# Kernel optimization log

Hardware: AMD Instinct MI355X
Metric: run time of the kernel (lower is better)

Reference implementation:

```python
import jax, jax.numpy as jnp
import numpy as np

H = 1024        # hidden_dim
NH = 8          # num_heads
HD = H // NH    # head_dim
EPS = 1e-5


def setup_inputs() -> dict:
    key = jax.random.key(0)
    ks = jax.random.split(key, 16)
    s = 0.02
    d = {
        'x': jax.random.normal(ks[0], (2, 2048, H), dtype=jnp.float32),
        'ln1_g': jnp.ones((H,), jnp.float32), 'ln1_b': jnp.zeros((H,), jnp.float32),
        'ln2_g': jnp.ones((H,), jnp.float32), 'ln2_b': jnp.zeros((H,), jnp.float32),
        'Wq': jax.random.normal(ks[1], (H, H), jnp.float32) * s,
        'bq': jnp.zeros((H,), jnp.float32),
        'Wk': jax.random.normal(ks[2], (H, H), jnp.float32) * s,
        'bk': jnp.zeros((H,), jnp.float32),
        'Wv': jax.random.normal(ks[3], (H, H), jnp.float32) * s,
        'bv': jnp.zeros((H,), jnp.float32),
        'Wo': jax.random.normal(ks[4], (H, H), jnp.float32) * s,
        'bo': jnp.zeros((H,), jnp.float32),
        'W1': jax.random.normal(ks[5], (H, 4 * H), jnp.float32) * s,
        'b1': jnp.zeros((4 * H,), jnp.float32),
        'W2': jax.random.normal(ks[6], (4 * H, H), jnp.float32) * s,
        'b2': jnp.zeros((H,), jnp.float32),
    }
    return d


def _layernorm(x, g, b):
    mu = jnp.mean(x, axis=-1, keepdims=True)
    var = jnp.mean(jnp.square(x - mu), axis=-1, keepdims=True)
    return (x - mu) * jax.lax.rsqrt(var + EPS) * g + b


def _block(x, ln1_g, ln1_b, ln2_g, ln2_b, Wq, bq, Wk, bk, Wv, bv, Wo, bo, W1, b1, W2, b2):
    B, S, _ = x.shape
    h = _layernorm(x, ln1_g, ln1_b)
    q = (h @ Wq + bq).reshape(B, S, NH, HD).transpose(0, 2, 1, 3)  # [B,NH,S,HD]
    k = (h @ Wk + bk).reshape(B, S, NH, HD).transpose(0, 2, 1, 3)
    v = (h @ Wv + bv).reshape(B, S, NH, HD).transpose(0, 2, 1, 3)
    scores = jnp.einsum('bhqd,bhkd->bhqk', q, k) / np.sqrt(HD)
    causal = jnp.tril(jnp.ones((S, S), bool))
    scores = jnp.where(causal, scores, -jnp.inf)
    attn = jax.nn.softmax(scores, axis=-1)
    y = jnp.einsum('bhqk,bhkd->bhqd', attn, v).transpose(0, 2, 1, 3).reshape(B, S, H)
    x = x + y @ Wo + bo
    h2 = _layernorm(x, ln2_g, ln2_b)
    m = jax.nn.gelu(h2 @ W1 + b1, approximate=False) @ W2 + b2
    return x + m


def reference(x, ln1_g, ln1_b, ln2_g, ln2_b, Wq, bq, Wk, bk, Wv, bv, Wo, bo, W1, b1, W2, b2):
    return _block(x, ln1_g, ln1_b, ln2_g, ln2_b, Wq, bq, Wk, bk, Wv, bv, Wo, bo, W1, b1, W2, b2)
```

## Files before the change

kernel.cpp:

```cpp
#include <hip/hip_runtime.h>
#include <hip/hip_bf16.h>
#include <math.h>

using bf16 = __hip_bfloat16;
typedef __attribute__((ext_vector_type(8))) short short8v;
typedef __attribute__((ext_vector_type(4))) float f32x4;

#define DEV __device__ __forceinline__

DEV void load_lds16(const bf16* gsrc, bf16* ldst) {
  __builtin_amdgcn_global_load_lds((const __attribute__((address_space(1))) void*)gsrc,
                                   (__attribute__((address_space(3))) void*)ldst, 16, 0, 0);
}

DEV void swz8(int& bx, int& by, int gx, int gy) {
  const int n = gx * gy, c = n >> 3;
  int lin = bx + gx * by;
  lin = (lin & 7) * c + (lin >> 3);
  bx = lin % gx; by = lin / gx;
}

__global__ __launch_bounds__(256) void prep_kernel(
    const float* __restrict__ Wq, const float* __restrict__ Wk, const float* __restrict__ Wv,
    const float* __restrict__ Wo, const float* __restrict__ W1, const float* __restrict__ W2,
    bf16* __restrict__ WqT, bf16* __restrict__ WkT, bf16* __restrict__ WvT,
    bf16* __restrict__ WoT, bf16* __restrict__ W1T, bf16* __restrict__ W2T,
    const float* __restrict__ x, const float* __restrict__ ln1g, const float* __restrict__ ln1b,
    bf16* __restrict__ h) {
  __shared__ float tile[64][65];
  const int b = blockIdx.x;
  if (b >= 3072) {
    const int row = b - 3072, t = threadIdx.x;
    const float4 v = ((const float4*)(x + (size_t)row * 1024))[t];
    float s = v.x + v.y + v.z + v.w;
#pragma unroll
    for (int mm = 1; mm < 64; mm <<= 1) s += __shfl_xor(s, mm);
    __shared__ float r1[4], r2[4];
    if ((t & 63) == 0) r1[t >> 6] = s;
    __syncthreads();
    const float mean = (r1[0] + r1[1] + r1[2] + r1[3]) * (1.0f / 1024.0f);
    const float d0 = v.x - mean, d1 = v.y - mean, d2 = v.z - mean, d3 = v.w - mean;
    float s2 = d0 * d0 + d1 * d1 + d2 * d2 + d3 * d3;
#pragma unroll
    for (int mm = 1; mm < 64; mm <<= 1) s2 += __shfl_xor(s2, mm);
    if ((t & 63) == 0) r2[t >> 6] = s2;
    __syncthreads();
    const float var = (r2[0] + r2[1] + r2[2] + r2[3]) * (1.0f / 1024.0f);
    const float rinv = rsqrtf(var + 1e-5f);
    const int c = t * 4;
    bf16* o = h + (size_t)row * 1024 + c;
    o[0] = __float2bfloat16(d0 * rinv * ln1g[c + 0] + ln1b[c + 0]);
    o[1] = __float2bfloat16(d1 * rinv * ln1g[c + 1] + ln1b[c + 1]);
    o[2] = __float2bfloat16(d2 * rinv * ln1g[c + 2] + ln1b[c + 2]);
    o[3] = __float2bfloat16(d3 * rinv * ln1g[c + 3] + ln1b[c + 3]);
    return;
  }
  const float* W; bf16* WT; int K, N, n0, k0;
  if (b < 1024) {
    const int which = b >> 8, t = b & 255;
    W  = (which == 0) ? Wq  : (which == 1) ? Wk  : (which == 2) ? Wv  : Wo;
    WT = (which == 0) ? WqT : (which == 1) ? WkT : (which == 2) ? WvT : WoT;
    K = 1024; N = 1024; n0 = (t & 15) * 64; k0 = (t >> 4) * 64;
  } else if (b < 2048) {
    const int t = b - 1024;
    W = W1; WT = W1T; K = 1024; N = 4096; n0 = (t & 63) * 64; k0 = (t >> 6) * 64;
  } else {
    const int t = b - 2048;
    W = W2; WT = W2T; K = 4096; N = 1024; n0 = (t & 15) * 64; k0 = (t >> 4) * 64;
  }
  const int tx = threadIdx.x & 15, ty = threadIdx.x >> 4;
#pragma unroll
  for (int p = 0; p < 4; ++p) {
    int r = p * 16 + ty;
    float4 vv = *(const float4*)&W[(size_t)(k0 + r) * N + n0 + tx * 4];
    tile[r][tx * 4 + 0] = vv.x; tile[r][tx * 4 + 1] = vv.y;
    tile[r][tx * 4 + 2] = vv.z; tile[r][tx * 4 + 3] = vv.w;
  }
  __syncthreads();
#pragma unroll
  for (int p = 0; p < 4; ++p) {
    int n = p * 16 + ty;
    bf16* dst = WT + (size_t)(n0 + n) * K + k0 + tx * 4;
#pragma unroll
    for (int j = 0; j < 4; ++j) dst[j] = __float2bfloat16(tile[tx * 4 + j][n]);
  }
}

__global__ __launch_bounds__(256) void ln_kernel(const float* __restrict__ x,
                                                 const float* __restrict__ g,
                                                 const float* __restrict__ b,
                                                 bf16* __restrict__ out) {
  const int row = blockIdx.x, t = threadIdx.x;
  const float4 v = ((const float4*)(x + (size_t)row * 1024))[t];
  float s = v.x + v.y + v.z + v.w;
#pragma unroll
  for (int mm = 1; mm < 64; mm <<= 1) s += __shfl_xor(s, mm);
  __shared__ float r1[4], r2[4];
  if ((t & 63) == 0) r1[t >> 6] = s;
  __syncthreads();
  const float mean = (r1[0] + r1[1] + r1[2] + r1[3]) * (1.0f / 1024.0f);
  const float d0 = v.x - mean, d1 = v.y - mean, d2 = v.z - mean, d3 = v.w - mean;
  float s2 = d0 * d0 + d1 * d1 + d2 * d2 + d3 * d3;
#pragma unroll
  for (int mm = 1; mm < 64; mm <<= 1) s2 += __shfl_xor(s2, mm);
  if ((t & 63) == 0) r2[t >> 6] = s2;
  __syncthreads();
  const float var = (r2[0] + r2[1] + r2[2] + r2[3]) * (1.0f / 1024.0f);
  const float rinv = rsqrtf(var + 1e-5f);
  const int c = t * 4;
  bf16* o = out + (size_t)row * 1024 + c;
  o[0] = __float2bfloat16(d0 * rinv * g[c + 0] + b[c + 0]);
  o[1] = __float2bfloat16(d1 * rinv * g[c + 1] + b[c + 1]);
  o[2] = __float2bfloat16(d2 * rinv * g[c + 2] + b[c + 2]);
  o[3] = __float2bfloat16(d3 * rinv * g[c + 3] + b[c + 3]);
}

template <int EPI>
__global__ __launch_bounds__(512, 2) void gemm256(
    const bf16* __restrict__ A, const bf16* __restrict__ BT,
    const float* __restrict__ bias0, const float* __restrict__ bias1, const float* __restrict__ bias2,
    void* __restrict__ outp, int M, int N, int K) {
  __shared__ bf16 As[4][256 * 32];
  __shared__ bf16 Bs[4][256 * 32];
  const int tid = threadIdx.x;
  const int w = tid >> 6, l = tid & 63;
  const int wm = w >> 2, wn = w & 3;
  const int c = l & 15, h4 = l >> 4;
  int bx = blockIdx.x, by = blockIdx.y;
  swz8(bx, by, gridDim.x, gridDim.y);
  const int m0 = by * 256, n0 = bx * 256;

  const float* bias;
  int zz = 0;
  if (EPI == 0) {
    zz = n0 >> 10;
    bias = ((zz == 0) ? bias0 : (zz == 1) ? bias1 : bias2) - (zz << 10);
  } else {
    bias = bias0;
  }

  const int rl = l >> 2;
  const int ch = (l & 3) * 8;
  const int nkt = K >> 5;

  f32x4 acc[8][4] = {};

  auto STAGE_A = [&](int t, int b) {
    const bf16* src = A + (size_t)(m0 + rl) * K + t * 32 + ch;
    load_lds16(src + (size_t)((w * 2 + 0) * 16) * K, &As[b][(w * 2 + 0) * 512]);
    load_lds16(src + (size_t)((w * 2 + 1) * 16) * K, &As[b][(w * 2 + 1) * 512]);
  };
  auto STAGE_B = [&](int t, int b) {
    const bf16* src = BT + (size_t)(n0 + rl) * K + t * 32 + ch;
    load_lds16(src + (size_t)((w * 2 + 0) * 16) * K, &Bs[b][(w * 2 + 0) * 512]);
    load_lds16(src + (size_t)((w * 2 + 1) * 16) * K, &Bs[b][(w * 2 + 1) * 512]);
  };

  STAGE_A(0, 0); STAGE_B(0, 0);
  STAGE_A(1, 1); STAGE_B(1, 1);
  STAGE_A(2, 2); STAGE_B(2, 2);
  asm volatile("s_waitcnt vmcnt(8)" ::: "memory");
  __builtin_amdgcn_sched_barrier(0);
  __builtin_amdgcn_s_barrier();

  for (int t = 0; t < nkt; ++t) {
    const bf16* Ab = &As[t & 3][0];
    const bf16* Bb = &Bs[t & 3][0];
    short8v a[4], b[4];
#pragma unroll
    for (int i = 0; i < 4; ++i)
      a[i] = *(const short8v*)&Ab[(wm * 128 + i * 16 + c) * 32 + h4 * 8];
#pragma unroll
    for (int i = 0; i < 4; ++i)
      b[i] = *(const short8v*)&Bb[(wn * 64 + i * 16 + c) * 32 + h4 * 8];
    if (t + 3 < nkt) STAGE_A(t + 3, (t + 3) & 3);
    asm volatile("s_waitcnt lgkmcnt(0)" ::: "memory");
    __builtin_amdgcn_sched_barrier(0);
    __builtin_amdgcn_s_setprio(1);
#pragma unroll
    for (int mi = 0; mi < 4; ++mi)
#pragma unroll
      for (int ni = 0; ni < 4; ++ni)
        acc[mi][ni] = __builtin_amdgcn_mfma_f32_16x16x32_bf16(a[mi], b[ni], acc[mi][ni], 0, 0, 0);
    __builtin_amdgcn_s_setprio(0);
#pragma unroll
    for (int i = 0; i < 4; ++i)
      a[i] = *(const short8v*)&Ab[(wm * 128 + 64 + i * 16 + c) * 32 + h4 * 8];
    if (t + 3 < nkt) STAGE_B(t + 3, (t + 3) & 3);
    asm volatile("s_waitcnt lgkmcnt(0)" ::: "memory");
    __builtin_amdgcn_sched_barrier(0);
    __builtin_amdgcn_s_setprio(1);
#pragma unroll
    for (int mi = 0; mi < 4; ++mi)
#pragma unroll
      for (int ni = 0; ni < 4; ++ni)
        acc[4 + mi][ni] = __builtin_amdgcn_mfma_f32_16x16x32_bf16(a[mi], b[ni], acc[4 + mi][ni], 0, 0, 0);
    __builtin_amdgcn_s_setprio(0);
    if (t < nkt - 3)       asm volatile("s_waitcnt vmcnt(8)" ::: "memory");
    else if (t == nkt - 3) asm volatile("s_waitcnt vmcnt(4)" ::: "memory");
    else                   asm volatile("s_waitcnt vmcnt(0)" ::: "memory");
    __builtin_amdgcn_sched_barrier(0);
    __builtin_amdgcn_s_barrier();
  }

#pragma unroll
  for (int mi = 0; mi < 8; ++mi) {
#pragma unroll
    for (int ni = 0; ni < 4; ++ni) {
#pragma unroll
      for (int r = 0; r < 4; ++r) {
        const int m = m0 + wm * 128 + mi * 16 + h4 * 4 + r;
        const int n = n0 + wn * 64 + ni * 16 + c;
        const float vv = acc[mi][ni][r] + bias[n];
        if (EPI == 0) {
          const int bb = m >> 11, ss = m & 2047;
          const int n1 = n - (zz << 10);
          const int hh = n1 >> 7, dd = n1 & 127;
          ((bf16*)outp)[(size_t)zz * 4194304 + (((size_t)bb * 8 + hh) * 2048 + ss) * 128 + dd] =
              __float2bfloat16(vv);
        } else {
          const size_t idx = (size_t)m * N + n;
          const float u = 0.7978845608028654f * (vv + 0.044715f * vv * vv * vv);
          const float tt = __expf(2.0f * u);
          const float th = 1.0f - 2.0f / (tt + 1.0f);
          ((bf16*)outp)[idx] = __float2bfloat16(0.5f * vv * (1.0f + th));
        }
      }
    }
  }
}

template <int EPI, int MI>
__global__ __launch_bounds__(256) void gemm128(
    const bf16* __restrict__ A, const bf16* __restrict__ BT,
    const float* __restrict__ bias0, const float* __restrict__ bias1, const float* __restrict__ bias2,
    const float* __restrict__ res, void* __restrict__ outp,
    int M, int N, int K) {
  __shared__ bf16 As[2][MI * 1024];
  __shared__ bf16 Bs[2][128 * 32];
  const int tid = threadIdx.x;
  const int w = tid >> 6, l = tid & 63;
  const int wr = w >> 1, wc = w & 1;
  const int col = l & 15, hi = l >> 4;
  int bx = blockIdx.x, by = blockIdx.y;
  swz8(bx, by, gridDim.x, gridDim.y);
  const int m0 = by * (32 * MI), n0 = bx * 128;

  const float* bias = bias0;

  const int srow = l >> 2;
  const int scol = ((l & 3) ^ ((l >> 4) & 3)) * 8;
  const int rs = col * 4 + (hi ^ ((l >> 2) & 3));
  f32x4 acc[MI][4] = {};

  const int nk = K >> 5;
#pragma unroll
  for (int j = 0; j < MI / 2; ++j) {
    const int grp = w * (MI / 2) + j;
    load_lds16(A + (size_t)(m0 + grp * 16 + srow) * K + scol, &As[0][grp * 512]);
  }
#pragma unroll
  for (int j = 0; j < 2; ++j) {
    const int grp = w * 2 + j;
    load_lds16(BT + (size_t)(n0 + grp * 16 + srow) * K + scol, &Bs[0][grp * 512]);
  }
  __syncthreads();

  int cur = 0;
  for (int kt = 0; kt < nk; ++kt) {
    if (kt + 1 < nk) {
      const int k0n = (kt + 1) * 32;
#pragma unroll
      for (int j = 0; j < MI / 2; ++j) {
        const int grp = w * (MI / 2) + j;
        load_lds16(A + (size_t)(m0 + grp * 16 + srow) * K + k0n + scol, &As[cur ^ 1][grp * 512]);
      }
#pragma unroll
      for (int j = 0; j < 2; ++j) {
        const int grp = w * 2 + j;
        load_lds16(BT + (size_t)(n0 + grp * 16 + srow) * K + k0n + scol, &Bs[cur ^ 1][grp * 512]);
      }
    }
    __builtin_amdgcn_sched_barrier(0);

    short8v af[MI], bfr[4];
#pragma unroll
    for (int i = 0; i < MI; ++i)
      af[i] = *(const short8v*)&As[cur][(wr * MI + i) * 512 + rs * 8];
#pragma unroll
    for (int i = 0; i < 4; ++i)
      bfr[i] = *(const short8v*)&Bs[cur][(wc * 4 + i) * 512 + rs * 8];
#pragma unroll
    for (int mi = 0; mi < MI; ++mi)
#pragma unroll
      for (int ni = 0; ni < 4; ++ni)
        acc[mi][ni] = __builtin_amdgcn_mfma_f32_16x16x32_bf16(af[mi], bfr[ni], acc[mi][ni], 0, 0, 0);
    __syncthreads();
    cur ^= 1;
  }

#pragma unroll
  for (int mi = 0; mi < MI; ++mi) {
#pragma unroll
    for (int ni = 0; ni < 4; ++ni) {
#pragma unroll
      for (int r = 0; r < 4; ++r) {
        const int m = m0 + wr * (16 * MI) + mi * 16 + hi * 4 + r;
        const int n = n0 + wc * 64 + ni * 16 + col;
        const float vv = acc[mi][ni][r] + bias[n];
        const size_t idx = (size_t)m * N + n;
        ((float*)outp)[idx] = res[idx] + vv;
      }
    }
  }
}

__global__ __launch_bounds__(512) void gemm_sk(
    const bf16* __restrict__ A, const bf16* __restrict__ BT,
    const float* __restrict__ bias, const float* __restrict__ res, float* __restrict__ outp,
    int M, int N, int K) {
  __shared__ bf16 As[2][2][4096];
  __shared__ bf16 Bs[2][2][4096];
  __shared__ float dump[128 * 132];
  const int tid = threadIdx.x;
  const int w = tid >> 6, l = tid & 63;
  const int grp = w >> 2, wg = w & 3;
  const int wr = wg >> 1, wc = wg & 1;
  const int col = l & 15, hi = l >> 4;
  int bx = blockIdx.x, by = blockIdx.y;
  swz8(bx, by, gridDim.x, gridDim.y);
  const int m0 = by * 128, n0 = bx * 128;

  const int srow = l >> 2;
  const int scol = ((l & 3) ^ ((l >> 4) & 3)) * 8;
  const int rs = col * 4 + (hi ^ ((l >> 2) & 3));
  f32x4 acc[4][4] = {};

  const int KH = K >> 1;
  const int kbase = grp * KH;
  const int nk = KH >> 5;

#pragma unroll
  for (int j = 0; j < 2; ++j) {
    const int rg = wg * 2 + j;
    load_lds16(A + (size_t)(m0 + rg * 16 + srow) * K + kbase + scol, &As[grp][0][rg * 512]);
    load_lds16(BT + (size_t)(n0 + rg * 16 + srow) * K + kbase + scol, &Bs[grp][0][rg * 512]);
  }
  __syncthreads();

  int cur = 0;
  for (int kt = 0; kt < nk; ++kt) {
    if (kt + 1 < nk) {
      const int k0n = kbase + (kt + 1) * 32;
#pragma unroll
      for (int j = 0; j < 2; ++j) {
        const int rg = wg * 2 + j;
        load_lds16(A + (size_t)(m0 + rg * 16 + srow) * K + k0n + scol, &As[grp][cur ^ 1][rg * 512]);
        load_lds16(BT + (size_t)(n0 + rg * 16 + srow) * K + k0n + scol, &Bs[grp][cur ^ 1][rg * 512]);
      }
    }
    __builtin_amdgcn_sched_barrier(0);

    short8v af[4], bfr[4];
#pragma unroll
    for (int i = 0; i < 4; ++i) {
      af[i]  = *(const short8v*)&As[grp][cur][(wr * 4 + i) * 512 + rs * 8];
      bfr[i] = *(const short8v*)&Bs[grp][cur][(wc * 4 + i) * 512 + rs * 8];
    }
#pragma unroll
    for (int mi = 0; mi < 4; ++mi)
#pragma unroll
      for (int ni = 0; ni < 4; ++ni)
        acc[mi][ni] = __builtin_amdgcn_mfma_f32_16x16x32_bf16(af[mi], bfr[ni], acc[mi][ni], 0, 0, 0);
    __syncthreads();
    cur ^= 1;
  }

  if (grp == 1) {
#pragma unroll
    for (int mi = 0; mi < 4; ++mi)
#pragma unroll
      for (int ni = 0; ni < 4; ++ni)
#pragma unroll
        for (int r = 0; r < 4; ++r)
          dump[(wr * 64 + mi * 16 + hi * 4 + r) * 132 + wc * 64 + ni * 16 + col] = acc[mi][ni][r];
  }
  __syncthreads();
  if (grp == 0) {
#pragma unroll
    for (int mi = 0; mi < 4; ++mi) {
#pragma unroll
      for (int ni = 0; ni < 4; ++ni) {
#pragma unroll
        for (int r = 0; r < 4; ++r) {
          const int lrow = wr * 64 + mi * 16 + hi * 4 + r;
          const int lcol = wc * 64 + ni * 16 + col;
          const int m = m0 + lrow, n = n0 + lcol;
          const size_t idx = (size_t)m * N + n;
          outp[idx] = res[idx] + acc[mi][ni][r] + dump[lrow * 132 + lcol] + bias[n];
        }
      }
    }
  }
}

__global__ __launch_bounds__(512) void attn_kernel(const bf16* __restrict__ q,
                                                   const bf16* __restrict__ k,
                                                   const bf16* __restrict__ v,
                                                   bf16* __restrict__ y) {
  __shared__ __align__(16) char lds_raw[157696];
  int p = blockIdx.x, bh = blockIdx.y;
  swz8(p, bh, 16, 16);
  const int tid = threadIdx.x;
  const int w = tid >> 6, l = tid & 63;
  const int grp = w >> 2, wg = w & 3;
  const int col = l & 15, hi = l >> 4;

  const bf16* kbase = k + (size_t)bh * 2048 * 128;
  const bf16* vbase = v + (size_t)bh * 2048 * 128;
  const int bb = bh >> 3, hh = bh & 7;

  bf16* Psw = (bf16*)(lds_raw + 139264 + (size_t)w * 2304);

  const int klr = (l >> 4);
  const int kblk0 = l & 15;
  const int vr = (l & 31) * 2;
  const int vcb = (wg * 2 + (l >> 5)) * 16;

  const float scale = 0.08838834764831845f;

  for (int half = 0; half < 2; ++half) {
    const int qt = half ? p : (31 - p);
    const int q0 = qt * 64;
    const int T = qt + 1;
    const int n0 = (T + 1) >> 1;
    const int myn = grp ? (T >> 1) : n0;
    const int tb = grp ? n0 : 0;

    short8v qf[4];
    const bf16* qp = q + ((size_t)bh * 2048 + q0 + wg * 16 + col) * 128;
#pragma unroll
    for (int c = 0; c < 4; ++c) qf[c] = *(const short8v*)(qp + c * 32 + hi * 8);

    f32x4 o[8] = {};
    float mx[4] = {-1e30f, -1e30f, -1e30f, -1e30f};
    float sm[4] = {0.f, 0.f, 0.f, 0.f};

    if (myn > 0) {
      bf16* Ks0 = (bf16*)(lds_raw + (size_t)(grp * 2 + 0) * 16384);
      bf16* Vt0 = (bf16*)(lds_raw + 65536 + (size_t)(grp * 2 + 0) * 18432);
#pragma unroll
      for (int j = 0; j < 4; ++j) {
        const int lr = j * 4 + klr;
        const int blk = kblk0 ^ (lr & 7);
        load_lds16(kbase + (size_t)(tb * 64 + wg * 16 + lr) * 128 + blk * 8,
                   Ks0 + wg * 2048 + j * 512);
      }
      const bf16* vsrc = vbase + (size_t)(tb * 64 + vr) * 128 + vcb;
      short8v v00 = *(const short8v*)vsrc;
      short8v v01 = *(const short8v*)(vsrc + 8);
      short8v v10 = *(const short8v*)(vsrc + 128);
      short8v v11 = *(const short8v*)(vsrc + 136);
#pragma unroll
      for (int i = 0; i < 8; ++i) {
        *(unsigned int*)&Vt0[(vcb + i) * 72 + vr] =
            ((unsigned int)(unsigned short)v00[i]) | (((unsigned int)(unsigned short)v10[i]) << 16);
        *(unsigned int*)&Vt0[(vcb + 8 + i) * 72 + vr] =
            ((unsigned int)(unsigned short)v01[i]) | (((unsigned int)(unsigned short)v11[i]) << 16);
      }
    }
    __syncthreads();

    for (int it = 0; it < n0; ++it) {
      const int cur = it & 1;
      const bool active = it < myn;
      const bool havenext = (it + 1) < myn;
      bf16* KsCur = (bf16*)(lds_raw + (size_t)(grp * 2 + cur) * 16384);
      bf16* KsNxt = (bf16*)(lds_raw + (size_t)(grp * 2 + (cur ^ 1)) * 16384);
      bf16* VtCur = (bf16*)(lds_raw + 65536 + (size_t)(grp * 2 + cur) * 18432);
      bf16* VtNxt = (bf16*)(lds_raw + 65536 + (size_t)(grp * 2 + (cur ^ 1)) * 18432);

      short8v v00, v01, v10, v11;
      if (havenext) {
        const int nt = tb + it + 1;
#pragma unroll
        for (int j = 0; j < 4; ++j) {
          const int lr = j * 4 + klr;
          const int blk = kblk0 ^ (lr & 7);
          load_lds16(kbase + (size_t)(nt * 64 + wg * 16 + lr) * 128 + blk * 8,
                     KsNxt + wg * 2048 + j * 512);
        }
        const bf16* vsrc = vbase + (size_t)(nt * 64 + vr) * 128 + vcb;
        v00 = *(const short8v*)vsrc;
        v01 = *(const short8v*)(vsrc + 8);
        v10 = *(const short8v*)(vsrc + 128);
        v11 = *(const short8v*)(vsrc + 136);
      }

      if (active) {
        const int ktile = tb + it;
        f32x4 s[4] = {};
        __builtin_amdgcn_s_setprio(1);
#pragma unroll
        for (int c = 0; c < 4; ++c) {
#pragma unroll
          for (int kg = 0; kg < 4; ++kg) {
            const int kr = kg * 16 + col;
            short8v kf = *(const short8v*)&KsCur[kr * 128 + ((c * 32 + hi * 8) ^ ((col & 7) << 3))];
            s[kg] = __builtin_amdgcn_mfma_f32_16x16x32_bf16(qf[c], kf, s[kg], 0, 0, 0);
          }
        }
        __builtin_amdgcn_s_setprio(0);

        const bool diag = (ktile == qt);
        const int qrl = wg * 16 + hi * 4;
        float al[4];
#pragma unroll
        for (int r = 0; r < 4; ++r) {
          float a0 = s[0][r] * scale, a1 = s[1][r] * scale;
          float a2 = s[2][r] * scale, a3 = s[3][r] * scale;
          if (diag) {
            const int qr = qrl + r;
            if (0 * 16 + col > qr) a0 = -1e30f;
            if (1 * 16 + col > qr) a1 = -1e30f;
            if (2 * 16 + col > qr) a2 = -1e30f;
            if (3 * 16 + col > qr) a3 = -1e30f;
          }
          float t = fmaxf(fmaxf(a0, a1), fmaxf(a2, a3));
#pragma unroll
          for (int mm = 1; mm < 16; mm <<= 1) t = fmaxf(t, __shfl_xor(t, mm));
          const float mn = fmaxf(mx[r], t);
          const float aa = __expf(mx[r] - mn);
          const float p0 = __expf(a0 - mn), p1 = __expf(a1 - mn);
          const float p2 = __expf(a2 - mn), p3 = __expf(a3 - mn);
          float ps = (p0 + p1) + (p2 + p3);
#pragma unroll
          for (int mm = 1; mm < 16; mm <<= 1) ps += __shfl_xor(ps, mm);
          sm[r] = sm[r] * aa + ps;
          mx[r] = mn; al[r] = aa;
          const int prow = (hi * 4 + r) * 72;
          Psw[prow + col]      = __float2bfloat16(p0);
          Psw[prow + col + 16] = __float2bfloat16(p1);
          Psw[prow + col + 32] = __float2bfloat16(p2);
          Psw[prow + col + 48] = __float2bfloat16(p3);
        }
#pragma unroll
        for (int db = 0; db < 8; ++db)
#pragma unroll
          for (int r = 0; r < 4; ++r) o[db][r] *= al[r];
      }

      if (havenext) {
#pragma unroll
        for (int i = 0; i < 8; ++i) {
          *(unsigned int*)&VtNxt[(vcb + i) * 72 + vr] =
              ((unsigned int)(unsigned short)v00[i]) | (((unsigned int)(unsigned short)v10[i]) << 16);
          *(unsigned int*)&VtNxt[(vcb + 8 + i) * 72 + vr] =
              ((unsigned int)(unsigned short)v01[i]) | (((unsigned int)(unsigned short)v11[i]) << 16);
        }
      }

      if (active) {
        asm volatile("s_waitcnt lgkmcnt(0)" ::: "memory");
        __builtin_amdgcn_s_setprio(1);
#pragma unroll
        for (int ks = 0; ks < 2; ++ks) {
          short8v pf = *(const short8v*)&Psw[col * 72 + ks * 32 + hi * 8];
#pragma unroll
          for (int db = 0; db < 8; ++db) {
            short8v vf = *(const short8v*)&VtCur[(db * 16 + col) * 72 + ks * 32 + hi * 8];
            o[db] = __builtin_amdgcn_mfma_f32_16x16x32_bf16(pf, vf, o[db], 0, 0, 0);
          }
        }
        __builtin_amdgcn_s_setprio(0);
      }
      __syncthreads();
    }

    if (grp == 1) {
      float* Mo = (float*)(lds_raw + (size_t)wg * 8448);
      float* Ml = (float*)(lds_raw + 33792 + (size_t)wg * 128);
#pragma unroll
      for (int db = 0; db < 8; ++db)
#pragma unroll
        for (int r = 0; r < 4; ++r)
          Mo[(hi * 4 + r) * 132 + db * 16 + col] = o[db][r];
#pragma unroll
      for (int r = 0; r < 4; ++r) {
        Ml[(hi * 4 + r) * 2 + 0] = mx[r];
        Ml[(hi * 4 + r) * 2 + 1] = sm[r];
      }
    }
    __syncthreads();
    if (grp == 0) {
      const float* Mo = (const float*)(lds_raw + (size_t)wg * 8448);
      const float* Ml = (const float*)(lds_raw + 33792 + (size_t)wg * 128);
      float a0[4], a1[4], inv[4];
#pragma unroll
      for (int r = 0; r < 4; ++r) {
        const float m1 = Ml[(hi * 4 + r) * 2 + 0];
        const float l1 = Ml[(hi * 4 + r) * 2 + 1];
        const float M = fmaxf(mx[r], m1);
        a0[r] = __expf(mx[r] - M);
        a1[r] = __expf(m1 - M);
        inv[r] = 1.0f / (sm[r] * a0[r] + l1 * a1[r]);
      }
#pragma unroll
      for (int db = 0; db < 8; ++db) {
#pragma unroll
        for (int r = 0; r < 4; ++r) {
          const float oc = o[db][r] * a0[r] + Mo[(hi * 4 + r) * 132 + db * 16 + col] * a1[r];
          const int qg = q0 + wg * 16 + hi * 4 + r;
          y[((size_t)bb * 2048 + qg) * 1024 + hh * 128 + db * 16 + col] =
              __float2bfloat16(oc * inv[r]);
        }
      }
    }
    __syncthreads();
  }
}

extern "C" void kernel_launch(void* const* d_in, const int* in_sizes, int n_in,
                              void* d_out, int out_size, void* d_ws, size_t ws_size,
                              hipStream_t stream) {
  const float* x    = (const float*)d_in[0];
  const float* ln1g = (const float*)d_in[1];
  const float* ln1b = (const float*)d_in[2];
  const float* ln2g = (const float*)d_in[3];
  const float* ln2b = (const float*)d_in[4];
  const float* Wq   = (const float*)d_in[5];
  const float* bq   = (const float*)d_in[6];
  const float* Wk   = (const float*)d_in[7];
  const float* bk   = (const float*)d_in[8];
  const float* Wv   = (const float*)d_in[9];
  const float* bv   = (const float*)d_in[10];
  const float* Wo   = (const float*)d_in[11];
  const float* bo   = (const float*)d_in[12];
  const float* W1   = (const float*)d_in[13];
  const float* b1   = (const float*)d_in[14];
  const float* W2   = (const float*)d_in[15];
  const float* b2   = (const float*)d_in[16];
  float* out = (float*)d_out;
  char* ws = (char*)d_ws;
  const size_t MB = 1024 * 1024;

  bf16* WqT = (bf16*)(ws + 0 * MB);
  bf16* WkT = (bf16*)(ws + 2 * MB);
  bf16* WvT = (bf16*)(ws + 4 * MB);
  bf16* WoT = (bf16*)(ws + 6 * MB);
  bf16* W1T = (bf16*)(ws + 8 * MB);
  bf16* W2T = (bf16*)(ws + 16 * MB);
  bf16* h   = (bf16*)(ws + 24 * MB);
  bf16* qb  = (bf16*)(ws + 32 * MB);
  bf16* kb  = (bf16*)(ws + 40 * MB);
  bf16* vb  = (bf16*)(ws + 48 * MB);
  bf16* y   = (bf16*)(ws + 56 * MB);
  bf16* g   = (bf16*)(ws + 32 * MB);
  float* x1 = (float*)(ws + 64 * MB);
  bf16* h2  = h;

  prep_kernel<<<7168, 256, 0, stream>>>(Wq, Wk, Wv, Wo, W1, W2, WqT, WkT, WvT, WoT, W1T, W2T,
                                        x, ln1g, ln1b, h);

  gemm256<0><<<dim3(12, 16), 512, 0, stream>>>(h, WqT, bq, bk, bv, qb, 4096, 3072, 1024);

  attn_kernel<<<dim3(16, 16), 512, 0, stream>>>(qb, kb, vb, y);

  gemm128<1, 2><<<dim3(8, 64), 256, 0, stream>>>(y, WoT, bo, nullptr, nullptr, x, x1,
                                                 4096, 1024, 1024);

  ln_kernel<<<4096, 256, 0, stream>>>(x1, ln2g, ln2b, h2);

  gemm256<2><<<dim3(16, 16), 512, 0, stream>>>(h2, W1T, b1, nullptr, nullptr, g,
                                               4096, 4096, 1024);

  gemm_sk<<<dim3(8, 32), 512, 0, stream>>>(g, W2T, b2, x1, out, 4096, 1024, 4096);
}
```

Baseline: 256.2 us.

## Deepen W2 split-K GEMM pipeline to four LDS stages with manual waitcnts

Rewrites the split-K down-projection GEMM so each K-group prefetches three tiles ahead into a four-deep LDS ring. Explicit vmcnt/lgkmcnt waits and raw s_barrier replace the per-iteration __syncthreads, and MFMA sections run at raised wave priority. The goal is to hide global-load latency better. In exchange it drops the XOR swizzle on LDS tiles, which may add bank conflicts, and uses 128KB of LDS, limiting occupancy to one block per CU.

```diff
diff --git a/kernel.cpp b/kernel.cpp
--- a/kernel.cpp
+++ b/kernel.cpp
@@ -315,13 +315,11 @@
   }
 }
 
-__global__ __launch_bounds__(512) void gemm_sk(
+__global__ __launch_bounds__(512, 1) void gemm_sk2(
     const bf16* __restrict__ A, const bf16* __restrict__ BT,
     const float* __restrict__ bias, const float* __restrict__ res, float* __restrict__ outp,
     int M, int N, int K) {
-  __shared__ bf16 As[2][2][4096];
-  __shared__ bf16 Bs[2][2][4096];
-  __shared__ float dump[128 * 132];
+  __shared__ __align__(16) char lds_raw[131072];
   const int tid = threadIdx.x;
   const int w = tid >> 6, l = tid & 63;
   const int grp = w >> 2, wg = w & 3;
@@ -331,51 +329,59 @@
   swz8(bx, by, gridDim.x, gridDim.y);
   const int m0 = by * 128, n0 = bx * 128;
 
-  const int srow = l >> 2;
-  const int scol = ((l & 3) ^ ((l >> 4) & 3)) * 8;
-  const int rs = col * 4 + (hi ^ ((l >> 2) & 3));
+  const int rl = l >> 2;
+  const int ch = (l & 3) * 8;
   f32x4 acc[4][4] = {};
 
   const int KH = K >> 1;
   const int kbase = grp * KH;
-  const int nk = KH >> 5;
-
-#pragma unroll
-  for (int j = 0; j < 2; ++j) {
-    const int rg = wg * 2 + j;
-    load_lds16(A + (size_t)(m0 + rg * 16 + srow) * K + kbase + scol, &As[grp][0][rg * 512]);
-    load_lds16(BT + (size_t)(n0 + rg * 16 + srow) * K + kbase + scol, &Bs[grp][0][rg * 512]);
-  }
-  __syncthreads();
-
-  int cur = 0;
-  for (int kt = 0; kt < nk; ++kt) {
-    if (kt + 1 < nk) {
-      const int k0n = kbase + (kt + 1) * 32;
-#pragma unroll
-      for (int j = 0; j < 2; ++j) {
-        const int rg = wg * 2 + j;
-        load_lds16(A + (size_t)(m0 + rg * 16 + srow) * K + k0n + scol, &As[grp][cur ^ 1][rg * 512]);
-        load_lds16(BT + (size_t)(n0 + rg * 16 + srow) * K + k0n + scol, &Bs[grp][cur ^ 1][rg * 512]);
-      }
-    }
+  const int nkt = KH >> 5;
+
+  auto ABUF = [&](int b) { return (bf16*)(lds_raw + grp * 65536 + b * 16384); };
+  auto BBUF = [&](int b) { return (bf16*)(lds_raw + grp * 65536 + b * 16384 + 8192); };
+
+  auto STAGE = [&](int t, int b) {
+    const bf16* srcA = A + (size_t)(m0 + rl) * K + kbase + t * 32 + ch;
+    const bf16* srcB = BT + (size_t)(n0 + rl) * K + kbase + t * 32 + ch;
+    bf16* Ab = ABUF(b); bf16* Bb = BBUF(b);
+    load_lds16(srcA + (size_t)((wg * 2 + 0) * 16) * K, Ab + (wg * 2 + 0) * 512);
+    load_lds16(srcA + (size_t)((wg * 2 + 1) * 16) * K, Ab + (wg * 2 + 1) * 512);
+    load_lds16(srcB + (size_t)((wg * 2 + 0) * 16) * K, Bb + (wg * 2 + 0) * 512);
+    load_lds16(srcB + (size_t)((wg * 2 + 1) * 16) * K, Bb + (wg * 2 + 1) * 512);
+  };
+
+  STAGE(0, 0); STAGE(1, 1); STAGE(2, 2);
+  asm volatile("s_waitcnt vmcnt(8)" ::: "memory");
+  __builtin_amdgcn_sched_barrier(0);
+  __builtin_amdgcn_s_barrier();
+
+  for (int t = 0; t < nkt; ++t) {
+    const bf16* Ab = ABUF(t & 3);
+    const bf16* Bb = BBUF(t & 3);
+    short8v af[4], bf_[4];
+#pragma unroll
+    for (int i = 0; i < 4; ++i) {
+      af[i]  = *(const short8v*)&Ab[(wr * 64 + i * 16 + col) * 32 + hi * 8];
+      bf_[i] = *(const short8v*)&Bb[(wc * 64 + i * 16 + col) * 32 + hi * 8];
+    }
+    if (t + 3 < nkt) STAGE(t + 3, (t + 3) & 3);
+    asm volatile("s_waitcnt lgkmcnt(0)" ::: "memory");
     __builtin_amdgcn_sched_barrier(0);
-
-    short8v af[4], bfr[4];
-#pragma unroll
-    for (int i = 0; i < 4; ++i) {
-      af[i]  = *(const short8v*)&As[grp][cur][(wr * 4 + i) * 512 + rs * 8];
-      bfr[i] = *(const short8v*)&Bs[grp][cur][(wc * 4 + i) * 512 + rs * 8];
-    }
+    __builtin_amdgcn_s_setprio(1);
 #pragma unroll
     for (int mi = 0; mi < 4; ++mi)
 #pragma unroll
       for (int ni = 0; ni < 4; ++ni)
-        acc[mi][ni] = __builtin_amdgcn_mfma_f32_16x16x32_bf16(af[mi], bfr[ni], acc[mi][ni], 0, 0, 0);
-    __syncthreads();
-    cur ^= 1;
-  }
-
+        acc[mi][ni] = __builtin_amdgcn_mfma_f32_16x16x32_bf16(af[mi], bf_[ni], acc[mi][ni], 0, 0, 0);
+    __builtin_amdgcn_s_setprio(0);
+    if (t < nkt - 3)       asm volatile("s_waitcnt vmcnt(8)" ::: "memory");
+    else if (t == nkt - 3) asm volatile("s_waitcnt vmcnt(4)" ::: "memory");
+    else                   asm volatile("s_waitcnt vmcnt(0)" ::: "memory");
+    __builtin_amdgcn_sched_barrier(0);
+    __builtin_amdgcn_s_barrier();
+  }
+
+  float* dump = (float*)lds_raw;
   if (grp == 1) {
 #pragma unroll
     for (int mi = 0; mi < 4; ++mi)
@@ -383,7 +389,7 @@
       for (int ni = 0; ni < 4; ++ni)
 #pragma unroll
         for (int r = 0; r < 4; ++r)
-          dump[(wr * 64 + mi * 16 + hi * 4 + r) * 132 + wc * 64 + ni * 16 + col] = acc[mi][ni][r];
+          dump[(wr * 64 + mi * 16 + hi * 4 + r) * 130 + wc * 64 + ni * 16 + col] = acc[mi][ni][r];
   }
   __syncthreads();
   if (grp == 0) {
@@ -397,7 +403,7 @@
           const int lcol = wc * 64 + ni * 16 + col;
           const int m = m0 + lrow, n = n0 + lcol;
           const size_t idx = (size_t)m * N + n;
-          outp[idx] = res[idx] + acc[mi][ni][r] + dump[lrow * 132 + lcol] + bias[n];
+          outp[idx] = res[idx] + acc[mi][ni][r] + dump[lrow * 130 + lcol] + bias[n];
         }
       }
     }
@@ -456,7 +462,7 @@
         load_lds16(kbase + (size_t)(tb * 64 + wg * 16 + lr) * 128 + blk * 8,
                    Ks0 + wg * 2048 + j * 512);
       }
-      const bf16* vsrc = vbase + (size_t)(tb * 64 + vr) * 128 + vcb;
+      const bf16* vsrc = vbase + (size_t)vr * 128 + vcb + (size_t)tb * 64 * 128;
       short8v v00 = *(const short8v*)vsrc;
       short8v v01 = *(const short8v*)(vsrc + 8);
       short8v v10 = *(const short8v*)(vsrc + 128);
@@ -674,5 +680,5 @@
   gemm256<2><<<dim3(16, 16), 512, 0, stream>>>(h2, W1T, b1, nullptr, nullptr, g,
                                                4096, 4096, 1024);
 
-  gemm_sk<<<dim3(8, 32), 512, 0, stream>>>(g, W2T, b2, x1, out, 4096, 1024, 4096);
-}
+  gemm_sk2<<<dim3(8, 32), 512, 0, stream>>>(g, W2T, b2, x1, out, 4096, 1024, 4096);
+}
```

After: 235.3 us. 1.09x faster.
